# Optimization experiments

Measured on AMD Instinct MI355X. Metric: run time of the kernel, lower is better.

## Reference

```python
import jax, jax.numpy as jnp
import numpy as np

N_NODES = 50000
N_EDGES = 800000
IN_FEATS, HIDDEN, OUT_FEATS = 512, 256, 128


def setup_inputs() -> dict:
    key = jax.random.key(0)
    ks = jax.random.split(key, 5)
    features = jax.random.normal(ks[0], (N_NODES, IN_FEATS), dtype=jnp.float32)
    W1 = jax.random.normal(ks[1], (IN_FEATS, HIDDEN), dtype=jnp.float32) * (1.0 / np.sqrt(IN_FEATS))
    b1 = jnp.zeros((HIDDEN,), dtype=jnp.float32)
    W2 = jax.random.normal(ks[2], (HIDDEN, OUT_FEATS), dtype=jnp.float32) * (1.0 / np.sqrt(HIDDEN))
    b2 = jnp.zeros((OUT_FEATS,), dtype=jnp.float32)
    src = jax.random.randint(ks[3], (N_EDGES,), 0, N_NODES, dtype=jnp.int32)
    dst = jax.random.randint(ks[4], (N_EDGES,), 0, N_NODES, dtype=jnp.int32)
    return {"features": features, "W1": W1, "b1": b1, "W2": W2, "b2": b2,
            "src": src, "dst": dst}


def reference(features, W1, b1, W2, b2, src, dst):
    # Two-layer GCN with DGL GraphConv norm='both':
    #   h = D_in^{-1/2} A D_out^{-1/2} (X W) + b
    N = features.shape[0]
    ones = jnp.ones(src.shape[0], dtype=features.dtype)
    deg_out = jnp.clip(jax.ops.segment_sum(ones, src, num_segments=N), 1.0)  # out-degree of src nodes
    deg_in = jnp.clip(jax.ops.segment_sum(ones, dst, num_segments=N), 1.0)   # in-degree of dst nodes
    norm_src = jax.lax.rsqrt(deg_out)[:, None]  # [N,1]
    norm_dst = jax.lax.rsqrt(deg_in)[:, None]   # [N,1]

    def gconv(x, W, b):
        h = (x * norm_src) @ W                                   # [N,d_out] weight first (in>out path)
        agg = jax.ops.segment_sum(h[src], dst, num_segments=N)   # sparse neighbor aggregation
        return agg * norm_dst + b

    h = jax.nn.relu(gconv(features, W1, b1))
    return gconv(h, W2, b2)
```

## Files before the change

kernel.cpp:

```cpp
#include <hip/hip_runtime.h>
#include <cstdint>
#include <cstddef>

#define NN 50000
#define NE 800000
static constexpr int IN_F = 512;
static constexpr int HID  = 256;
static constexpr int OUTF = 128;

typedef __attribute__((ext_vector_type(8))) _Float16 half8;
typedef __attribute__((ext_vector_type(4))) _Float16 half4v;
typedef __attribute__((ext_vector_type(2))) _Float16 half2v;
typedef __attribute__((ext_vector_type(4))) float f32x4;


__global__ void k_degree(const int* __restrict__ src, const int* __restrict__ dst,
                         int* __restrict__ deg_out, int* __restrict__ deg_in, int E) {
  int e = blockIdx.x * blockDim.x + threadIdx.x;
  if (e < E) {
    atomicAdd(&deg_out[src[e]], 1);
    atomicAdd(&deg_in[dst[e]], 1);
  }
}

__global__ void k_norm(const int* __restrict__ deg_out, const int* __restrict__ deg_in,
                       float* __restrict__ norm_src, float* __restrict__ norm_dst, int N) {
  int i = blockIdx.x * blockDim.x + threadIdx.x;
  if (i < N) {
    int dO = deg_out[i]; if (dO < 1) dO = 1;
    int dI = deg_in[i];  if (dI < 1) dI = 1;
    norm_src[i] = rsqrtf((float)dO);
    norm_dst[i] = rsqrtf((float)dI);
  }
}

__global__ void k_scan1(const int* __restrict__ deg_in, int* __restrict__ excl,
                        int* __restrict__ bsums, int N) {
  __shared__ int s[512];
  int t = threadIdx.x;
  int g = blockIdx.x * 512 + t;
  int v = (g < N) ? deg_in[g] : 0;
  s[t] = v;
  __syncthreads();
  for (int off = 1; off < 512; off <<= 1) {
    int add = (t >= off) ? s[t - off] : 0;
    __syncthreads();
    s[t] += add;
    __syncthreads();
  }
  if (g < N) excl[g] = s[t] - v;
  if (t == 511) bsums[blockIdx.x] = s[511];
}

__global__ void k_scan2(int* __restrict__ bsums, int nb) {
  __shared__ int s[128];
  int t = threadIdx.x;
  int v = (t < nb) ? bsums[t] : 0;
  s[t] = v;
  __syncthreads();
  for (int off = 1; off < 128; off <<= 1) {
    int add = (t >= off) ? s[t - off] : 0;
    __syncthreads();
    s[t] += add;
    __syncthreads();
  }
  if (t < nb) bsums[t] = s[t] - v;
}

__global__ void k_scan3(int* __restrict__ row_off, const int* __restrict__ bsums,
                        int N, int E) {
  int g = blockIdx.x * blockDim.x + threadIdx.x;
  if (g < N) row_off[g] += bsums[g >> 9];
  if (g == 0) row_off[N] = E;
}

__global__ void k_fill(const int* __restrict__ src, const int* __restrict__ dst,
                       const int* __restrict__ row_off, int* __restrict__ cursor,
                       int* __restrict__ ssrc, int E) {
  int e = blockIdx.x * blockDim.x + threadIdx.x;
  if (e < E) {
    int d = dst[e];
    int pos = atomicAdd(&cursor[d], 1);
    ssrc[row_off[d] + pos] = src[e];
  }
}

__global__ void k_convW(const float* __restrict__ W, _Float16* __restrict__ WT,
                        int K, int N) {
  int t = blockIdx.x * blockDim.x + threadIdx.x;
  if (t >= K * N) return;
  int n = t / K, k = t - n * K;
  WT[t] = (_Float16)W[(size_t)k * N + n];
}

template <bool AF32, bool SCALE>
__launch_bounds__(256)
__global__ void k_gemm_f16(const void* __restrict__ Ap,
                           const _Float16* __restrict__ BT,
                           const float* __restrict__ rowscale,
                           _Float16* __restrict__ C, int M, int N, int K) {
  __shared__ uint4 sA[2][512];
  __shared__ uint4 sB[2][512];

  const int tid = threadIdx.x;
  const int wid = tid >> 6, lane = tid & 63;
  const int bm = blockIdx.x * 128, bn = blockIdx.y * 128;
  const int wrow = wid >> 1, wcol = wid & 1;

  const _Float16* Af16 = (const _Float16*)Ap;
  const float* Af32 = (const float*)Ap;

  const int c0 = tid, c1 = 256 + tid;
  const float *pa0 = nullptr, *pa1 = nullptr;
  float sc0 = 1.f, sc1 = 1.f;
  if constexpr (AF32) {
    const int f0 = c0 >> 6, r0 = c0 & 63;
    const int f1 = c1 >> 6, r1 = c1 & 63;
    int g0 = bm + f0 * 16 + (r0 & 15); if (g0 > M - 1) g0 = M - 1;
    int g1 = bm + f1 * 16 + (r1 & 15); if (g1 > M - 1) g1 = M - 1;
    if constexpr (SCALE) { sc0 = rowscale[g0]; sc1 = rowscale[g1]; }
    pa0 = Af32 + (size_t)g0 * K + (r0 >> 4) * 8;
    pa1 = Af32 + (size_t)g1 * K + (r1 >> 4) * 8;
  }

  float4 av[4];
  auto loadA32 = [&](int k0) {
    av[0] = *(const float4*)(pa0 + k0);
    av[1] = *(const float4*)(pa0 + k0 + 4);
    av[2] = *(const float4*)(pa1 + k0);
    av[3] = *(const float4*)(pa1 + k0 + 4);
  };
  auto cvtWriteA = [&](int buf) {
#pragma unroll
    for (int j = 0; j < 2; ++j) {
      const float s = j ? sc1 : sc0;
      const float4 u = av[j * 2], v = av[j * 2 + 1];
      float fv[8] = {u.x, u.y, u.z, u.w, v.x, v.y, v.z, v.w};
      union { _Float16 h[8]; uint4 q; } pk;
#pragma unroll
      for (int i = 0; i < 8; ++i)
        pk.h[i] = (_Float16)(SCALE ? fv[i] * s : fv[i]);
      sA[buf][j ? c1 : c0] = pk.q;
    }
  };
  auto stageA16 = [&](int buf, int k0) {
#pragma unroll
    for (int i = 0; i < 2; ++i) {
      const int f = wid * 2 + i;
      int g = bm + f * 16 + (lane & 15); if (g > M - 1) g = M - 1;
      const _Float16* s = Af16 + (size_t)g * K + k0 + (lane >> 4) * 8;
      __builtin_amdgcn_global_load_lds(
          (const __attribute__((address_space(1))) unsigned int*)s,
          (__attribute__((address_space(3))) unsigned int*)&sA[buf][f * 64], 16, 0, 0);
    }
  };
  auto stageB = [&](int buf, int k0) {
#pragma unroll
    for (int i = 0; i < 2; ++i) {
      const int f = wid * 2 + i;
      const _Float16* s = BT + (size_t)(bn + f * 16 + (lane & 15)) * K + k0 + (lane >> 4) * 8;
      __builtin_amdgcn_global_load_lds(
          (const __attribute__((address_space(1))) unsigned int*)s,
          (__attribute__((address_space(3))) unsigned int*)&sB[buf][f * 64], 16, 0, 0);
    }
  };

  f32x4 acc[4][4] = {};
  auto mfmaPhase = [&](int buf) {
    half8 ah[4], bh[4];
#pragma unroll
    for (int m = 0; m < 4; ++m)
      ah[m] = *(const half8*)&sA[buf][(wrow * 4 + m) * 64 + lane];
#pragma unroll
    for (int n = 0; n < 4; ++n)
      bh[n] = *(const half8*)&sB[buf][(wcol * 4 + n) * 64 + lane];
#pragma unroll
    for (int m = 0; m < 4; ++m)
#pragma unroll
      for (int n = 0; n < 4; ++n)
        acc[m][n] = __builtin_amdgcn_mfma_f32_16x16x32_f16(ah[m], bh[n], acc[m][n], 0, 0, 0);
  };

  const int nt = K >> 5;
  if constexpr (AF32) loadA32(0); else stageA16(0, 0);
  stageB(0, 0);
  if constexpr (AF32) cvtWriteA(0);
  __syncthreads();
  for (int t = 0; t < nt; ++t) {
    const int cur = t & 1;
    const bool more = (t + 1 < nt);
    if (more) {
      if constexpr (AF32) loadA32((t + 1) << 5); else stageA16(cur ^ 1, (t + 1) << 5);
      stageB(cur ^ 1, (t + 1) << 5);
    }
    mfmaPhase(cur);
    if (more) { if constexpr (AF32) cvtWriteA(cur ^ 1); }
    __syncthreads();
  }

#pragma unroll
  for (int m = 0; m < 4; ++m) {
    const int rb = bm + wrow * 64 + m * 16 + (lane >> 4) * 4;
#pragma unroll
    for (int r = 0; r < 4; ++r) {
      const int gm = rb + r;
      if (gm < M) {
        _Float16* cp = C + (size_t)gm * N + bn + wcol * 64 + (lane & 15);
#pragma unroll
        for (int n = 0; n < 4; ++n) cp[n * 16] = (_Float16)acc[m][n][r];
      }
    }
  }
}

template <int F, bool RELU, bool OSCALE, bool OUT16>
__launch_bounds__(256)
__global__ void k_agg16(const _Float16* __restrict__ H, const int* __restrict__ row_off,
                        const int* __restrict__ ssrc, const float* __restrict__ norm_dst,
                        const float* __restrict__ bias, const float* __restrict__ oscale,
                        void* __restrict__ outp, int N) {
  int wid = (blockIdx.x * 256 + threadIdx.x) >> 6;
  int lane = threadIdx.x & 63;
  if (wid >= N) return;
  int beg = row_off[wid], end = row_off[wid + 1];
  float nd = norm_dst[wid];

  if constexpr (F == 256) {
    float a0[4] = {}, a1[4] = {}, a2[4] = {}, a3[4] = {};
    int e = beg;
    for (; e + 4 <= end; e += 4) {
      int s0 = ssrc[e], s1 = ssrc[e + 1], s2 = ssrc[e + 2], s3 = ssrc[e + 3];
      half4v v0 = *(const half4v*)(H + (size_t)s0 * 256 + lane * 4);
      half4v v1 = *(const half4v*)(H + (size_t)s1 * 256 + lane * 4);
      half4v v2 = *(const half4v*)(H + (size_t)s2 * 256 + lane * 4);
      half4v v3 = *(const half4v*)(H + (size_t)s3 * 256 + lane * 4);
#pragma unroll
      for (int i = 0; i < 4; ++i) {
        a0[i] += (float)v0[i]; a1[i] += (float)v1[i];
        a2[i] += (float)v2[i]; a3[i] += (float)v3[i];
      }
    }
    for (; e < end; ++e) {
      half4v v = *(const half4v*)(H + (size_t)ssrc[e] * 256 + lane * 4);
#pragma unroll
      for (int i = 0; i < 4; ++i) a0[i] += (float)v[i];
    }
    const float4 bb = *(const float4*)(bias + lane * 4);
    float bv[4] = {bb.x, bb.y, bb.z, bb.w};
    float o[4];
#pragma unroll
    for (int i = 0; i < 4; ++i) {
      o[i] = fmaf(a0[i] + a1[i] + a2[i] + a3[i], nd, bv[i]);
      if (RELU) o[i] = fmaxf(o[i], 0.f);
    }
    if (OSCALE) {
      float os = oscale[wid];
#pragma unroll
      for (int i = 0; i < 4; ++i) o[i] *= os;
    }
    if constexpr (OUT16) {
      union { _Float16 h[4]; uint2 q; } pk;
#pragma unroll
      for (int i = 0; i < 4; ++i) pk.h[i] = (_Float16)o[i];
      *(uint2*)((_Float16*)outp + (size_t)wid * 256 + lane * 4) = pk.q;
    } else {
      *(float4*)((float*)outp + (size_t)wid * 256 + lane * 4) =
          make_float4(o[0], o[1], o[2], o[3]);
    }
  } else {
    float a0[2] = {}, a1[2] = {}, a2[2] = {}, a3[2] = {};
    int e = beg;
    for (; e + 4 <= end; e += 4) {
      int s0 = ssrc[e], s1 = ssrc[e + 1], s2 = ssrc[e + 2], s3 = ssrc[e + 3];
      half2v v0 = *(const half2v*)(H + (size_t)s0 * 128 + lane * 2);
      half2v v1 = *(const half2v*)(H + (size_t)s1 * 128 + lane * 2);
      half2v v2 = *(const half2v*)(H + (size_t)s2 * 128 + lane * 2);
      half2v v3 = *(const half2v*)(H + (size_t)s3 * 128 + lane * 2);
#pragma unroll
      for (int i = 0; i < 2; ++i) {
        a0[i] += (float)v0[i]; a1[i] += (float)v1[i];
        a2[i] += (float)v2[i]; a3[i] += (float)v3[i];
      }
    }
    for (; e < end; ++e) {
      half2v v = *(const half2v*)(H + (size_t)ssrc[e] * 128 + lane * 2);
#pragma unroll
      for (int i = 0; i < 2; ++i) a0[i] += (float)v[i];
    }
    const float2 bb = *(const float2*)(bias + lane * 2);
    float bv[2] = {bb.x, bb.y};
    float o[2];
#pragma unroll
    for (int i = 0; i < 2; ++i) {
      o[i] = fmaf(a0[i] + a1[i] + a2[i] + a3[i], nd, bv[i]);
      if (RELU) o[i] = fmaxf(o[i], 0.f);
    }
    if (OSCALE) {
      float os = oscale[wid];
#pragma unroll
      for (int i = 0; i < 2; ++i) o[i] *= os;
    }
    if constexpr (OUT16) {
      union { _Float16 h[2]; unsigned q; } pk;
      pk.h[0] = (_Float16)o[0]; pk.h[1] = (_Float16)o[1];
      *(unsigned*)((_Float16*)outp + (size_t)wid * 128 + lane * 2) = pk.q;
    } else {
      *(float2*)((float*)outp + (size_t)wid * 128 + lane * 2) = make_float2(o[0], o[1]);
    }
  }
}


extern "C" void kernel_launch(void* const* d_in, const int* in_sizes, int n_in,
                              void* d_out, int out_size, void* d_ws, size_t ws_size,
                              hipStream_t stream) {
  const float* X  = (const float*)d_in[0];
  const float* W1 = (const float*)d_in[1];
  const float* b1 = (const float*)d_in[2];
  const float* W2 = (const float*)d_in[3];
  const float* b2 = (const float*)d_in[4];
  const int* src  = (const int*)d_in[5];
  const int* dst  = (const int*)d_in[6];
  float* out = (float*)d_out;

  char* p = (char*)d_ws;
  auto alloc = [&](size_t bytes) -> char* {
    char* r = p;
    p += (bytes + 255) & ~(size_t)255;
    return r;
  };
  _Float16* H1pre  = (_Float16*)alloc((size_t)NN * HID * 2);
  _Float16* H1post = (_Float16*)alloc((size_t)NN * HID * 2);
  _Float16* H2pre  = H1pre;
  _Float16* W1T = (_Float16*)alloc((size_t)HID * IN_F * 2);
  _Float16* W2T = (_Float16*)alloc((size_t)OUTF * HID * 2);
  int* deg_out  = (int*)alloc((size_t)NN * 4);
  int* deg_in   = (int*)alloc((size_t)NN * 4);
  int* cursor   = (int*)alloc((size_t)NN * 4);
  int* row_off  = (int*)alloc((size_t)(NN + 1) * 4);
  int* bsums    = (int*)alloc(512);
  float* nsrc   = (float*)alloc((size_t)NN * 4);
  float* ndst   = (float*)alloc((size_t)NN * 4);
  int* ssrc     = (int*)alloc((size_t)NE * 4);

  hipMemsetAsync(deg_out, 0, (size_t)((char*)row_off - (char*)deg_out), stream);

  k_degree<<<(NE + 255) / 256, 256, 0, stream>>>(src, dst, deg_out, deg_in, NE);
  k_norm<<<(NN + 255) / 256, 256, 0, stream>>>(deg_out, deg_in, nsrc, ndst, NN);

  int nb = (NN + 511) / 512;
  k_scan1<<<nb, 512, 0, stream>>>(deg_in, row_off, bsums, NN);
  k_scan2<<<1, 128, 0, stream>>>(bsums, nb);
  k_scan3<<<(NN + 255) / 256, 256, 0, stream>>>(row_off, bsums, NN, NE);
  k_fill<<<(NE + 255) / 256, 256, 0, stream>>>(src, dst, row_off, cursor, ssrc, NE);

  k_convW<<<(IN_F * HID + 255) / 256, 256, 0, stream>>>(W1, W1T, IN_F, HID);
  k_convW<<<(HID * OUTF + 255) / 256, 256, 0, stream>>>(W2, W2T, HID, OUTF);

  dim3 g1((NN + 127) / 128, HID / 128);
  k_gemm_f16<true, true><<<g1, 256, 0, stream>>>(X, W1T, nsrc, H1pre, NN, HID, IN_F);
  k_agg16<256, true, true, true><<<(NN * 64 + 255) / 256, 256, 0, stream>>>(
      H1pre, row_off, ssrc, ndst, b1, nsrc, H1post, NN);

  dim3 g2((NN + 127) / 128, OUTF / 128);
  k_gemm_f16<false, false><<<g2, 256, 0, stream>>>(H1post, W2T, nullptr, H2pre, NN, OUTF, HID);
  k_agg16<128, false, false, false><<<(NN * 64 + 255) / 256, 256, 0, stream>>>(
      H2pre, row_off, ssrc, ndst, b2, nullptr, out, NN);
}
```

Measured before the change: 423.1 us.

## Pre-convert scaled X to fp16 and use async LDS loads with K=64 tiles in GEMM

```diff
diff --git a/kernel.cpp b/kernel.cpp
--- a/kernel.cpp
+++ b/kernel.cpp
@@ -85,6 +85,22 @@
   }
 }
 
+__global__ void k_convX(const float* __restrict__ X, const float* __restrict__ nsrc,
+                        _Float16* __restrict__ Xh) {
+  const int t = blockIdx.x * 256 + threadIdx.x;
+  const int base = t * 8;
+  const int m = base >> 9;
+  const float s = nsrc[m];
+  const float4 a = *(const float4*)(X + base);
+  const float4 b = *(const float4*)(X + base + 4);
+  union { _Float16 h[8]; uint4 q; } pk;
+  pk.h[0] = (_Float16)(a.x * s); pk.h[1] = (_Float16)(a.y * s);
+  pk.h[2] = (_Float16)(a.z * s); pk.h[3] = (_Float16)(a.w * s);
+  pk.h[4] = (_Float16)(b.x * s); pk.h[5] = (_Float16)(b.y * s);
+  pk.h[6] = (_Float16)(b.z * s); pk.h[7] = (_Float16)(b.w * s);
+  *(uint4*)(Xh + base) = pk.q;
+}
+
 __global__ void k_convW(const float* __restrict__ W, _Float16* __restrict__ WT,
                         int K, int N) {
   int t = blockIdx.x * blockDim.x + threadIdx.x;
@@ -93,108 +109,75 @@
   WT[t] = (_Float16)W[(size_t)k * N + n];
 }
 
-template <bool AF32, bool SCALE>
-__launch_bounds__(256)
-__global__ void k_gemm_f16(const void* __restrict__ Ap,
+template <int NT>
+__launch_bounds__(256, 2)
+__global__ void k_gemm_f16(const _Float16* __restrict__ A,
                            const _Float16* __restrict__ BT,
-                           const float* __restrict__ rowscale,
-                           _Float16* __restrict__ C, int M, int N, int K) {
-  __shared__ uint4 sA[2][512];
-  __shared__ uint4 sB[2][512];
+                           _Float16* __restrict__ C, int M, int N) {
+  constexpr int K = NT * 64;
+  __shared__ uint4 sA[2][16 * 64];
+  __shared__ uint4 sB[2][16 * 64];
 
   const int tid = threadIdx.x;
   const int wid = tid >> 6, lane = tid & 63;
   const int bm = blockIdx.x * 128, bn = blockIdx.y * 128;
   const int wrow = wid >> 1, wcol = wid & 1;
 
-  const _Float16* Af16 = (const _Float16*)Ap;
-  const float* Af32 = (const float*)Ap;
-
-  const int c0 = tid, c1 = 256 + tid;
-  const float *pa0 = nullptr, *pa1 = nullptr;
-  float sc0 = 1.f, sc1 = 1.f;
-  if constexpr (AF32) {
-    const int f0 = c0 >> 6, r0 = c0 & 63;
-    const int f1 = c1 >> 6, r1 = c1 & 63;
-    int g0 = bm + f0 * 16 + (r0 & 15); if (g0 > M - 1) g0 = M - 1;
-    int g1 = bm + f1 * 16 + (r1 & 15); if (g1 > M - 1) g1 = M - 1;
-    if constexpr (SCALE) { sc0 = rowscale[g0]; sc1 = rowscale[g1]; }
-    pa0 = Af32 + (size_t)g0 * K + (r0 >> 4) * 8;
-    pa1 = Af32 + (size_t)g1 * K + (r1 >> 4) * 8;
-  }
-
-  float4 av[4];
-  auto loadA32 = [&](int k0) {
-    av[0] = *(const float4*)(pa0 + k0);
-    av[1] = *(const float4*)(pa0 + k0 + 4);
-    av[2] = *(const float4*)(pa1 + k0);
-    av[3] = *(const float4*)(pa1 + k0 + 4);
-  };
-  auto cvtWriteA = [&](int buf) {
-#pragma unroll
-    for (int j = 0; j < 2; ++j) {
-      const float s = j ? sc1 : sc0;
-      const float4 u = av[j * 2], v = av[j * 2 + 1];
-      float fv[8] = {u.x, u.y, u.z, u.w, v.x, v.y, v.z, v.w};
-      union { _Float16 h[8]; uint4 q; } pk;
-#pragma unroll
-      for (int i = 0; i < 8; ++i)
-        pk.h[i] = (_Float16)(SCALE ? fv[i] * s : fv[i]);
-      sA[buf][j ? c1 : c0] = pk.q;
-    }
-  };
-  auto stageA16 = [&](int buf, int k0) {
-#pragma unroll
-    for (int i = 0; i < 2; ++i) {
-      const int f = wid * 2 + i;
-      int g = bm + f * 16 + (lane & 15); if (g > M - 1) g = M - 1;
-      const _Float16* s = Af16 + (size_t)g * K + k0 + (lane >> 4) * 8;
+  auto stage = [&](int buf, int k0) {
+#pragma unroll
+    for (int i = 0; i < 4; ++i) {
+      const int fa = wid * 4 + i;
+      const int mf = fa >> 1, ks = fa & 1;
+      int g = bm + mf * 16 + (lane & 15); if (g > M - 1) g = M - 1;
+      const _Float16* s = A + (size_t)g * K + k0 + ks * 32 + (lane >> 4) * 8;
       __builtin_amdgcn_global_load_lds(
           (const __attribute__((address_space(1))) unsigned int*)s,
-          (__attribute__((address_space(3))) unsigned int*)&sA[buf][f * 64], 16, 0, 0);
-    }
-  };
-  auto stageB = [&](int buf, int k0) {
-#pragma unroll
-    for (int i = 0; i < 2; ++i) {
-      const int f = wid * 2 + i;
-      const _Float16* s = BT + (size_t)(bn + f * 16 + (lane & 15)) * K + k0 + (lane >> 4) * 8;
+          (__attribute__((address_space(3))) unsigned int*)&sA[buf][fa * 64], 16, 0, 0);
+    }
+#pragma unroll
+    for (int i = 0; i < 4; ++i) {
+      const int fb = wid * 4 + i;
+      const int nf = fb >> 1, ks = fb & 1;
+      const _Float16* s =
+          BT + (size_t)(bn + nf * 16 + (lane & 15)) * K + k0 + ks * 32 + (lane >> 4) * 8;
       __builtin_amdgcn_global_load_lds(
           (const __attribute__((address_space(1))) unsigned int*)s,
-          (__attribute__((address_space(3))) unsigned int*)&sB[buf][f * 64], 16, 0, 0);
+          (__attribute__((address_space(3))) unsigned int*)&sB[buf][fb * 64], 16, 0, 0);
     }
   };
 
   f32x4 acc[4][4] = {};
   auto mfmaPhase = [&](int buf) {
-    half8 ah[4], bh[4];
-#pragma unroll
-    for (int m = 0; m < 4; ++m)
-      ah[m] = *(const half8*)&sA[buf][(wrow * 4 + m) * 64 + lane];
-#pragma unroll
-    for (int n = 0; n < 4; ++n)
-      bh[n] = *(const half8*)&sB[buf][(wcol * 4 + n) * 64 + lane];
-#pragma unroll
-    for (int m = 0; m < 4; ++m)
-#pragma unroll
-      for (int n = 0; n < 4; ++n)
-        acc[m][n] = __builtin_amdgcn_mfma_f32_16x16x32_f16(ah[m], bh[n], acc[m][n], 0, 0, 0);
+#pragma unroll
+    for (int ks = 0; ks < 2; ++ks) {
+      half8 af[4], bf[4];
+#pragma unroll
+      for (int m = 0; m < 4; ++m) {
+        union { uint4 q; half8 h; } u;
+        u.q = sA[buf][((wrow * 4 + m) * 2 + ks) * 64 + lane];
+        af[m] = u.h;
+      }
+#pragma unroll
+      for (int n = 0; n < 4; ++n) {
+        union { uint4 q; half8 h; } u;
+        u.q = sB[buf][((wcol * 4 + n) * 2 + ks) * 64 + lane];
+        bf[n] = u.h;
+      }
+#pragma unroll
+      for (int m = 0; m < 4; ++m)
+#pragma unroll
+        for (int n = 0; n < 4; ++n)
+          acc[m][n] = __builtin_amdgcn_mfma_f32_16x16x32_f16(af[m], bf[n], acc[m][n], 0, 0, 0);
+    }
   };
 
-  const int nt = K >> 5;
-  if constexpr (AF32) loadA32(0); else stageA16(0, 0);
-  stageB(0, 0);
-  if constexpr (AF32) cvtWriteA(0);
+  stage(0, 0);
   __syncthreads();
-  for (int t = 0; t < nt; ++t) {
+#pragma unroll
+  for (int t = 0; t < NT; ++t) {
     const int cur = t & 1;
-    const bool more = (t + 1 < nt);
-    if (more) {
-      if constexpr (AF32) loadA32((t + 1) << 5); else stageA16(cur ^ 1, (t + 1) << 5);
-      stageB(cur ^ 1, (t + 1) << 5);
-    }
+    if (t + 1 < NT) stage(cur ^ 1, (t + 1) * 64);
     mfmaPhase(cur);
-    if (more) { if constexpr (AF32) cvtWriteA(cur ^ 1); }
     __syncthreads();
   }
 
@@ -329,6 +312,7 @@
     p += (bytes + 255) & ~(size_t)255;
     return r;
   };
+  _Float16* Xh     = (_Float16*)alloc((size_t)NN * IN_F * 2);
   _Float16* H1pre  = (_Float16*)alloc((size_t)NN * HID * 2);
   _Float16* H1post = (_Float16*)alloc((size_t)NN * HID * 2);
   _Float16* H2pre  = H1pre;
@@ -347,6 +331,7 @@
 
   k_degree<<<(NE + 255) / 256, 256, 0, stream>>>(src, dst, deg_out, deg_in, NE);
   k_norm<<<(NN + 255) / 256, 256, 0, stream>>>(deg_out, deg_in, nsrc, ndst, NN);
+  k_convX<<<(NN * IN_F / 8 + 255) / 256, 256, 0, stream>>>(X, nsrc, Xh);
 
   int nb = (NN + 511) / 512;
   k_scan1<<<nb, 512, 0, stream>>>(deg_in, row_off, bsums, NN);
@@ -358,12 +343,12 @@
   k_convW<<<(HID * OUTF + 255) / 256, 256, 0, stream>>>(W2, W2T, HID, OUTF);
 
   dim3 g1((NN + 127) / 128, HID / 128);
-  k_gemm_f16<true, true><<<g1, 256, 0, stream>>>(X, W1T, nsrc, H1pre, NN, HID, IN_F);
+  k_gemm_f16<IN_F / 64><<<g1, 256, 0, stream>>>(Xh, W1T, H1pre, NN, HID);
   k_agg16<256, true, true, true><<<(NN * 64 + 255) / 256, 256, 0, stream>>>(
       H1pre, row_off, ssrc, ndst, b1, nsrc, H1post, NN);
 
   dim3 g2((NN + 127) / 128, OUTF / 128);
-  k_gemm_f16<false, false><<<g2, 256, 0, stream>>>(H1post, W2T, nullptr, H2pre, NN, OUTF, HID);
+  k_gemm_f16<HID / 64><<<g2, 256, 0, stream>>>(H1post, W2T, H2pre, NN, OUTF);
   k_agg16<128, false, false, false><<<(NN * 64 + 255) / 256, 256, 0, stream>>>(
       H2pre, row_off, ssrc, ndst, b2, nullptr, out, NN);
 }
```

New measurement: 437.9 us. +3.5%, slower.
